# Kernel tuning notes

Measured on AMD Instinct MI355X. Metric: run time of the kernel, lower is better.

The kernel has to match this reference:

```python
import jax, jax.numpy as jnp
import numpy as np

N = 50000      # nodes
E = 200000     # edges per edge type (avg in-degree 16 over 4 etypes)
R = 4          # number of edge types
DIN = 128
DH = 128
DOUT = 64


def setup_inputs() -> dict:
    key = jax.random.key(0)
    ks = jax.random.split(key, 6)
    feat = jax.random.normal(ks[0], (N, DIN), dtype=jnp.float32)
    edges = jax.random.randint(ks[1], (R, 2, E), 0, N)  # [R, (src,dst), E]
    s1 = 1.0 / np.sqrt(DIN)
    W1 = jax.random.uniform(ks[2], (R, DIN, DH), jnp.float32, -s1, s1)
    b1 = jax.random.uniform(ks[3], (R, DH), jnp.float32, -s1, s1)
    s2 = 1.0 / np.sqrt(DH)
    W2 = jax.random.uniform(ks[4], (R, DH, DOUT), jnp.float32, -s2, s2)
    b2 = jax.random.uniform(ks[5], (R, DOUT), jnp.float32, -s2, s2)
    return {"feat": feat, "W1": W1, "b1": b1, "W2": W2, "b2": b2, "edges": edges}


def _hetero_layer(h, W, b, edges):
    """Per-etype Linear -> copy_u + mean over in-edges -> sum across etypes."""
    n = h.shape[0]

    def per_etype(Wr, br, er):
        Wh = h @ Wr + br                       # [N, d_out]
        src, dst = er[0], er[1]
        msg = Wh[src]                          # gather [E, d_out]
        ssum = jax.ops.segment_sum(msg, dst, num_segments=n)
        deg = jax.ops.segment_sum(jnp.ones((er.shape[1],), Wh.dtype), dst,
                                  num_segments=n)
        return ssum / jnp.maximum(deg, 1.0)[:, None]   # mean; 0 for isolated nodes

    return jax.vmap(per_etype)(W, b, edges).sum(axis=0)  # 'sum' cross reducer


def reference(feat, W1, b1, W2, b2, edges):
    h = _hetero_layer(feat, W1, b1, edges)
    h = jax.nn.relu(h)
    return _hetero_layer(h, W2, b2, edges)
```

## Files before the change

### kernel.cpp

```cpp
#include <hip/hip_runtime.h>

#define NN 50000
#define EE 200000
#define RR 4
#define SC_TOTAL (RR * NN)
#define CAP 32
#define GTILE ((NN + 127) / 128)
#define NB_G1 (4 * GTILE)
#define NB_F  1563

typedef __attribute__((ext_vector_type(8))) short bf16x8;
typedef __attribute__((ext_vector_type(4))) float f32x4;

__device__ inline unsigned short f2bf(float x) {
    unsigned int u = __float_as_uint(x);
    u += 0x7fffu + ((u >> 16) & 1u);
    return (unsigned short)(u >> 16);
}
__device__ inline float bflo(unsigned u) { return __uint_as_float(u << 16); }
__device__ inline float bfhi(unsigned u) { return __uint_as_float(u & 0xffff0000u); }

__global__ __launch_bounds__(256) void init_kernel(
    const float* __restrict__ feat, unsigned short* __restrict__ featb,
    const float* __restrict__ W1, const float* __restrict__ b1,
    const float* __restrict__ W2, const float* __restrict__ b2,
    unsigned short* __restrict__ W1T, unsigned short* __restrict__ W2T,
    float* __restrict__ btab1, float* __restrict__ btab2,
    int* __restrict__ cnt)
{
    int b = blockIdx.x, t = threadIdx.x;
    if (b < 6250) {
        int i = (b * 256 + t) * 4;
        float4 v = *(const float4*)&feat[i];
        unsigned lo = (unsigned)f2bf(v.x) | ((unsigned)f2bf(v.y) << 16);
        unsigned hi = (unsigned)f2bf(v.z) | ((unsigned)f2bf(v.w) << 16);
        *(uint2*)&featb[i] = make_uint2(lo, hi);
    } else if (b < 6506) {
        int i = (b - 6250) * 256 + t;
        int jout = i >> 7, k = i & 127;
        int r = jout >> 7, j = jout & 127;
        W1T[i] = f2bf(W1[r * 16384 + k * 128 + j]);
    } else if (b < 6634) {
        int i = (b - 6506) * 256 + t;
        int jout = i >> 7, k = i & 127;
        int r = jout >> 6, j = jout & 63;
        W2T[i] = f2bf(W2[r * 8192 + k * 64 + j]);
    } else if (b < 6642) {
        int i = (b - 6634) * 256 + t;
        int mm = i >> 7, c = i & 127;
        float s = 0.f;
        #pragma unroll
        for (int r = 0; r < RR; ++r) if (mm & (1 << r)) s += b1[r * 128 + c];
        btab1[i] = s;
    } else if (b < 6646) {
        int i = (b - 6642) * 256 + t;
        int mm = i >> 6, c = i & 63;
        float s = 0.f;
        #pragma unroll
        for (int r = 0; r < RR; ++r) if (mm & (1 << r)) s += b2[r * 64 + c];
        btab2[i] = s;
    } else {
        int i = ((b - 6646) * 256 + t) * 4;
        if (i < SC_TOTAL) *(int4*)&cnt[i] = make_int4(0, 0, 0, 0);
    }
}

__global__ __launch_bounds__(256) void fill_gemm1(
    const int* __restrict__ edges, int* __restrict__ cnt,
    unsigned short* __restrict__ ssrc2,
    const unsigned short* __restrict__ A, const unsigned short* __restrict__ WT,
    unsigned short* __restrict__ H)
{
    __shared__ __align__(16) unsigned short Wl[128 * 128];
    const int bid = blockIdx.x;
    const int tid = threadIdx.x;

    if (bid & 1) {
        int f = bid >> 1;
        #pragma unroll
        for (int k = 0; k < 2; ++k) {
            int i = f * 512 + k * 256 + tid;
            if (i < RR * EE) {
                int r = i / EE;
                int e = i - r * EE;
                const int* es = edges + (size_t)r * 2 * EE;
                int src = es[e];
                int dst = es[EE + e];
                int seg = r * NN + dst;
                int p = atomicAdd(&cnt[seg], 1);
                if (p < CAP) ssrc2[(size_t)seg * CAP + p] = (unsigned short)src;
            }
        }
        return;
    }

    const int g    = bid >> 1;
    const int wv   = tid >> 6;
    const int lane = tid & 63;
    const int m    = lane & 15;
    const int q    = lane >> 4;
    const int col0 = (g & 3) * 128;
    const int row0 = (g >> 2) * 128;

    #pragma unroll
    for (int i = 0; i < 8; ++i) {
        int L  = i * 4096 + tid * 16;
        int nr = L >> 8, ir = L & 255;
        uint4 v = *(const uint4*)((const char*)WT + ((size_t)(col0 + nr) << 8) + ir);
        *(uint4*)((char*)Wl + nr * 256 + (ir ^ ((nr & 7) << 4))) = v;
    }
    __syncthreads();

    f32x4 acc[2][8];
    #pragma unroll
    for (int rf = 0; rf < 2; ++rf)
        #pragma unroll
        for (int nt = 0; nt < 8; ++nt) acc[rf][nt] = (f32x4){0.f, 0.f, 0.f, 0.f};

    const int ra0 = row0 + wv * 32 + m;
    const int ra1 = ra0 + 16;
    const bool g0 = ra0 < NN, g1 = ra1 < NN;
    const unsigned short* Ap0 = A + (size_t)ra0 * 128 + q * 8;
    const unsigned short* Ap1 = A + (size_t)ra1 * 128 + q * 8;
    const bf16x8 bz = (bf16x8){0, 0, 0, 0, 0, 0, 0, 0};

    #pragma unroll
    for (int kk = 0; kk < 4; ++kk) {
        bf16x8 a0 = g0 ? *(const bf16x8*)(Ap0 + kk * 32) : bz;
        bf16x8 a1 = g1 ? *(const bf16x8*)(Ap1 + kk * 32) : bz;
        #pragma unroll
        for (int nt = 0; nt < 8; ++nt) {
            int offb = (nt * 16 + m) * 256 + ((kk * 64 + q * 16) ^ ((m & 7) << 4));
            bf16x8 bfr = *(const bf16x8*)((const char*)Wl + offb);
            acc[0][nt] = __builtin_amdgcn_mfma_f32_16x16x32_bf16(a0, bfr, acc[0][nt], 0, 0, 0);
            acc[1][nt] = __builtin_amdgcn_mfma_f32_16x16x32_bf16(a1, bfr, acc[1][nt], 0, 0, 0);
        }
    }

    #pragma unroll
    for (int rf = 0; rf < 2; ++rf) {
        #pragma unroll
        for (int rg = 0; rg < 4; ++rg) {
            int row = row0 + wv * 32 + rf * 16 + q * 4 + rg;
            if (row < NN) {
                unsigned short* Hp = H + (size_t)row * 512 + col0 + m;
                #pragma unroll
                for (int nt = 0; nt < 8; ++nt)
                    Hp[nt * 16] = f2bf(acc[rf][nt][rg]);
            }
        }
    }
}

template<int OTOT>
__global__ __launch_bounds__(256) void gemm_tf(
    const unsigned short* __restrict__ A, const unsigned short* __restrict__ WT,
    unsigned short* __restrict__ H)
{
    __shared__ __align__(16) unsigned short Wl[128 * 128];
    const int tid  = threadIdx.x;
    const int wv   = tid >> 6;
    const int lane = tid & 63;
    const int m    = lane & 15;
    const int q    = lane >> 4;
    const int col0 = blockIdx.x * 128;
    const int row0 = blockIdx.y * 128;

    #pragma unroll
    for (int i = 0; i < 8; ++i) {
        int L  = i * 4096 + tid * 16;
        int nr = L >> 8, ir = L & 255;
        uint4 v = *(const uint4*)((const char*)WT + ((size_t)(col0 + nr) << 8) + ir);
        *(uint4*)((char*)Wl + nr * 256 + (ir ^ ((nr & 7) << 4))) = v;
    }
    __syncthreads();

    f32x4 acc[2][8];
    #pragma unroll
    for (int rf = 0; rf < 2; ++rf)
        #pragma unroll
        for (int nt = 0; nt < 8; ++nt) acc[rf][nt] = (f32x4){0.f, 0.f, 0.f, 0.f};

    const int ra0 = row0 + wv * 32 + m;
    const int ra1 = ra0 + 16;
    const bool g0 = ra0 < NN, g1 = ra1 < NN;
    const unsigned short* Ap0 = A + (size_t)ra0 * 128 + q * 8;
    const unsigned short* Ap1 = A + (size_t)ra1 * 128 + q * 8;
    const bf16x8 bz = (bf16x8){0, 0, 0, 0, 0, 0, 0, 0};

    #pragma unroll
    for (int kk = 0; kk < 4; ++kk) {
        bf16x8 a0 = g0 ? *(const bf16x8*)(Ap0 + kk * 32) : bz;
        bf16x8 a1 = g1 ? *(const bf16x8*)(Ap1 + kk * 32) : bz;
        #pragma unroll
        for (int nt = 0; nt < 8; ++nt) {
            int offb = (nt * 16 + m) * 256 + ((kk * 64 + q * 16) ^ ((m & 7) << 4));
            bf16x8 bfr = *(const bf16x8*)((const char*)Wl + offb);
            acc[0][nt] = __builtin_amdgcn_mfma_f32_16x16x32_bf16(a0, bfr, acc[0][nt], 0, 0, 0);
            acc[1][nt] = __builtin_amdgcn_mfma_f32_16x16x32_bf16(a1, bfr, acc[1][nt], 0, 0, 0);
        }
    }

    #pragma unroll
    for (int rf = 0; rf < 2; ++rf) {
        #pragma unroll
        for (int rg = 0; rg < 4; ++rg) {
            int row = row0 + wv * 32 + rf * 16 + q * 4 + rg;
            if (row < NN) {
                unsigned short* Hp = H + (size_t)row * OTOT + col0 + m;
                #pragma unroll
                for (int nt = 0; nt < 8; ++nt)
                    Hp[nt * 16] = f2bf(acc[rf][nt][rg]);
            }
        }
    }
}

__global__ __launch_bounds__(256) void gather_node1(
    const unsigned short* __restrict__ H1, const unsigned short* __restrict__ ssrc2,
    const int* __restrict__ cnt, const float* __restrict__ btab1,
    unsigned short* __restrict__ h1r)
{
    int n = blockIdx.x * 16 + (threadIdx.x >> 4);
    if (n >= NN) return;
    int l = threadIdx.x & 15;
    float a0 = 0.f, a1 = 0.f, a2 = 0.f, a3 = 0.f, a4 = 0.f, a5 = 0.f, a6 = 0.f, a7 = 0.f;
    int mk = 0;
    #pragma unroll
    for (int r = 0; r < RR; ++r) {
        int seg = r * NN + n;
        int deg = cnt[seg];
        if (deg <= 0) continue;
        mk |= 1 << r;
        int nd = (deg < CAP) ? deg : CAP;
        const unsigned short* lst  = ssrc2 + (size_t)seg * CAP;
        const unsigned short* base = H1 + r * 128 + l * 8;
        float b0 = 0.f, b1v = 0.f, b2v = 0.f, b3 = 0.f, b4 = 0.f, b5 = 0.f, b6 = 0.f, b7 = 0.f;
        int j = 0;
        for (; j + 1 < nd; j += 2) {
            uint4 u0 = *(const uint4*)(base + (size_t)lst[j] * 512);
            uint4 u1 = *(const uint4*)(base + (size_t)lst[j + 1] * 512);
            b0 += bflo(u0.x) + bflo(u1.x); b1v += bfhi(u0.x) + bfhi(u1.x);
            b2v += bflo(u0.y) + bflo(u1.y); b3 += bfhi(u0.y) + bfhi(u1.y);
            b4 += bflo(u0.z) + bflo(u1.z); b5 += bfhi(u0.z) + bfhi(u1.z);
            b6 += bflo(u0.w) + bflo(u1.w); b7 += bfhi(u0.w) + bfhi(u1.w);
        }
        if (j < nd) {
            uint4 u0 = *(const uint4*)(base + (size_t)lst[j] * 512);
            b0 += bflo(u0.x); b1v += bfhi(u0.x);
            b2v += bflo(u0.y); b3 += bfhi(u0.y);
            b4 += bflo(u0.z); b5 += bfhi(u0.z);
            b6 += bflo(u0.w); b7 += bfhi(u0.w);
        }
        float inv = 1.0f / (float)deg;
        a0 += b0 * inv; a1 += b1v * inv; a2 += b2v * inv; a3 += b3 * inv;
        a4 += b4 * inv; a5 += b5 * inv; a6 += b6 * inv; a7 += b7 * inv;
    }
    const float* bt = btab1 + mk * 128 + l * 8;
    float4 t0 = *(const float4*)bt;
    float4 t1 = *(const float4*)(bt + 4);
    uint4 o;
    o.x = (unsigned)f2bf(fmaxf(a0 + t0.x, 0.f)) | ((unsigned)f2bf(fmaxf(a1 + t0.y, 0.f)) << 16);
    o.y = (unsigned)f2bf(fmaxf(a2 + t0.z, 0.f)) | ((unsigned)f2bf(fmaxf(a3 + t0.w, 0.f)) << 16);
    o.z = (unsigned)f2bf(fmaxf(a4 + t1.x, 0.f)) | ((unsigned)f2bf(fmaxf(a5 + t1.y, 0.f)) << 16);
    o.w = (unsigned)f2bf(fmaxf(a6 + t1.z, 0.f)) | ((unsigned)f2bf(fmaxf(a7 + t1.w, 0.f)) << 16);
    *(uint4*)&h1r[(size_t)n * 128 + l * 8] = o;
}

__global__ __launch_bounds__(256) void gather_node2(
    const unsigned short* __restrict__ H2, const unsigned short* __restrict__ ssrc2,
    const int* __restrict__ cnt, const float* __restrict__ btab2,
    float* __restrict__ out)
{
    int n = blockIdx.x * 32 + (threadIdx.x >> 3);
    if (n >= NN) return;
    int l = threadIdx.x & 7;
    float a0 = 0.f, a1 = 0.f, a2 = 0.f, a3 = 0.f, a4 = 0.f, a5 = 0.f, a6 = 0.f, a7 = 0.f;
    int mk = 0;
    #pragma unroll
    for (int r = 0; r < RR; ++r) {
        int seg = r * NN + n;
        int deg = cnt[seg];
        if (deg <= 0) continue;
        mk |= 1 << r;
        int nd = (deg < CAP) ? deg : CAP;
        const unsigned short* lst  = ssrc2 + (size_t)seg * CAP;
        const unsigned short* base = H2 + r * 64 + l * 8;
        float b0 = 0.f, b1v = 0.f, b2v = 0.f, b3 = 0.f, b4 = 0.f, b5 = 0.f, b6 = 0.f, b7 = 0.f;
        int j = 0;
        for (; j + 1 < nd; j += 2) {
            uint4 u0 = *(const uint4*)(base + (size_t)lst[j] * 256);
            uint4 u1 = *(const uint4*)(base + (size_t)lst[j + 1] * 256);
            b0 += bflo(u0.x) + bflo(u1.x); b1v += bfhi(u0.x) + bfhi(u1.x);
            b2v += bflo(u0.y) + bflo(u1.y); b3 += bfhi(u0.y) + bfhi(u1.y);
            b4 += bflo(u0.z) + bflo(u1.z); b5 += bfhi(u0.z) + bfhi(u1.z);
            b6 += bflo(u0.w) + bflo(u1.w); b7 += bfhi(u0.w) + bfhi(u1.w);
        }
        if (j < nd) {
            uint4 u0 = *(const uint4*)(base + (size_t)lst[j] * 256);
            b0 += bflo(u0.x); b1v += bfhi(u0.x);
            b2v += bflo(u0.y); b3 += bfhi(u0.y);
            b4 += bflo(u0.z); b5 += bfhi(u0.z);
            b6 += bflo(u0.w); b7 += bfhi(u0.w);
        }
        float inv = 1.0f / (float)deg;
        a0 += b0 * inv; a1 += b1v * inv; a2 += b2v * inv; a3 += b3 * inv;
        a4 += b4 * inv; a5 += b5 * inv; a6 += b6 * inv; a7 += b7 * inv;
    }
    const float* bt = btab2 + mk * 64 + l * 8;
    float4 t0 = *(const float4*)bt;
    float4 t1 = *(const float4*)(bt + 4);
    float* op = out + (size_t)n * 64 + l * 8;
    *(float4*)op       = make_float4(a0 + t0.x, a1 + t0.y, a2 + t0.z, a3 + t0.w);
    *(float4*)(op + 4) = make_float4(a4 + t1.x, a5 + t1.y, a6 + t1.z, a7 + t1.w);
}

extern "C" void kernel_launch(void* const* d_in, const int* in_sizes, int n_in,
                              void* d_out, int out_size, void* d_ws, size_t ws_size,
                              hipStream_t stream)
{
    const float* feat  = (const float*)d_in[0];
    const float* W1    = (const float*)d_in[1];
    const float* b1    = (const float*)d_in[2];
    const float* W2    = (const float*)d_in[3];
    const float* b2    = (const float*)d_in[4];
    const int*   edges = (const int*)d_in[5];
    float* out = (float*)d_out;

    char* p = (char*)d_ws;
    auto alloc = [&](size_t bytes) { char* q = p; p += (bytes + 255) & ~(size_t)255; return q; };
    int* cnt                 = (int*)alloc((size_t)SC_TOTAL * 4);
    unsigned short* ssrc2    = (unsigned short*)alloc((size_t)SC_TOTAL * CAP * 2);
    unsigned short* W1T      = (unsigned short*)alloc((size_t)512 * 128 * 2);
    unsigned short* W2T      = (unsigned short*)alloc((size_t)256 * 128 * 2);
    float* btab1             = (float*)alloc((size_t)16 * 128 * 4);
    float* btab2             = (float*)alloc((size_t)16 * 64 * 4);
    unsigned short* featb    = (unsigned short*)alloc((size_t)NN * 128 * 2);
    unsigned short* h1r      = (unsigned short*)alloc((size_t)NN * 128 * 2);
    unsigned short* H        = (unsigned short*)alloc((size_t)NN * 512 * 2);

    init_kernel<<<6842, 256, 0, stream>>>(feat, featb, W1, b1, W2, b2,
                                          W1T, W2T, btab1, btab2, cnt);
    fill_gemm1<<<NB_G1 + NB_F, 256, 0, stream>>>(edges, cnt, ssrc2, featb, W1T, H);
    gather_node1<<<(NN + 15) / 16, 256, 0, stream>>>(H, ssrc2, cnt, btab1, h1r);
    gemm_tf<256><<<dim3(2, GTILE), 256, 0, stream>>>(h1r, W2T, H);
    gather_node2<<<(NN + 31) / 32, 256, 0, stream>>>(H, ssrc2, cnt, btab2, out);
}
```

Measured before the change: 200.2 us.

## Fuse feat bf16 conversion into GEMM1 and batch-prefetch neighbor indices in gathers

Drops the separate fp32-to-bf16 pass over feat in init_kernel. The first GEMM now loads fp32 rows directly and packs them to bf16 in registers, which removes a full write and re-read of a 12.8MB buffer. The gather kernels now load each node's first 8 neighbor indices per edge type as one uint4 and issue the gathers for all four edge types in an interleaved unrolled loop, to expose more memory-level parallelism. A slower fallback loop handles degrees above 8, and the per-type accumulators raise register pressure.

```diff
diff --git a/kernel.cpp b/kernel.cpp
--- a/kernel.cpp
+++ b/kernel.cpp
@@ -20,8 +20,16 @@
 __device__ inline float bflo(unsigned u) { return __uint_as_float(u << 16); }
 __device__ inline float bfhi(unsigned u) { return __uint_as_float(u & 0xffff0000u); }
 
+__device__ inline bf16x8 pk8(float4 x, float4 y) {
+    bf16x8 o;
+    o[0] = (short)f2bf(x.x); o[1] = (short)f2bf(x.y);
+    o[2] = (short)f2bf(x.z); o[3] = (short)f2bf(x.w);
+    o[4] = (short)f2bf(y.x); o[5] = (short)f2bf(y.y);
+    o[6] = (short)f2bf(y.z); o[7] = (short)f2bf(y.w);
+    return o;
+}
+
 __global__ __launch_bounds__(256) void init_kernel(
-    const float* __restrict__ feat, unsigned short* __restrict__ featb,
     const float* __restrict__ W1, const float* __restrict__ b1,
     const float* __restrict__ W2, const float* __restrict__ b2,
     unsigned short* __restrict__ W1T, unsigned short* __restrict__ W2T,
@@ -29,38 +37,32 @@
     int* __restrict__ cnt)
 {
     int b = blockIdx.x, t = threadIdx.x;
-    if (b < 6250) {
-        int i = (b * 256 + t) * 4;
-        float4 v = *(const float4*)&feat[i];
-        unsigned lo = (unsigned)f2bf(v.x) | ((unsigned)f2bf(v.y) << 16);
-        unsigned hi = (unsigned)f2bf(v.z) | ((unsigned)f2bf(v.w) << 16);
-        *(uint2*)&featb[i] = make_uint2(lo, hi);
-    } else if (b < 6506) {
-        int i = (b - 6250) * 256 + t;
+    if (b < 256) {
+        int i = b * 256 + t;
         int jout = i >> 7, k = i & 127;
         int r = jout >> 7, j = jout & 127;
         W1T[i] = f2bf(W1[r * 16384 + k * 128 + j]);
-    } else if (b < 6634) {
-        int i = (b - 6506) * 256 + t;
+    } else if (b < 384) {
+        int i = (b - 256) * 256 + t;
         int jout = i >> 7, k = i & 127;
         int r = jout >> 6, j = jout & 63;
         W2T[i] = f2bf(W2[r * 8192 + k * 64 + j]);
-    } else if (b < 6642) {
-        int i = (b - 6634) * 256 + t;
+    } else if (b < 392) {
+        int i = (b - 384) * 256 + t;
         int mm = i >> 7, c = i & 127;
         float s = 0.f;
         #pragma unroll
         for (int r = 0; r < RR; ++r) if (mm & (1 << r)) s += b1[r * 128 + c];
         btab1[i] = s;
-    } else if (b < 6646) {
-        int i = (b - 6642) * 256 + t;
+    } else if (b < 396) {
+        int i = (b - 392) * 256 + t;
         int mm = i >> 6, c = i & 63;
         float s = 0.f;
         #pragma unroll
         for (int r = 0; r < RR; ++r) if (mm & (1 << r)) s += b2[r * 64 + c];
         btab2[i] = s;
     } else {
-        int i = ((b - 6646) * 256 + t) * 4;
+        int i = ((b - 396) * 256 + t) * 4;
         if (i < SC_TOTAL) *(int4*)&cnt[i] = make_int4(0, 0, 0, 0);
     }
 }
@@ -68,7 +70,7 @@
 __global__ __launch_bounds__(256) void fill_gemm1(
     const int* __restrict__ edges, int* __restrict__ cnt,
     unsigned short* __restrict__ ssrc2,
-    const unsigned short* __restrict__ A, const unsigned short* __restrict__ WT,
+    const float* __restrict__ feat, const unsigned short* __restrict__ WT,
     unsigned short* __restrict__ H)
 {
     __shared__ __align__(16) unsigned short Wl[128 * 128];
@@ -120,14 +122,23 @@
     const int ra0 = row0 + wv * 32 + m;
     const int ra1 = ra0 + 16;
     const bool g0 = ra0 < NN, g1 = ra1 < NN;
-    const unsigned short* Ap0 = A + (size_t)ra0 * 128 + q * 8;
-    const unsigned short* Ap1 = A + (size_t)ra1 * 128 + q * 8;
+    const float* Af0 = feat + (size_t)ra0 * 128 + q * 8;
+    const float* Af1 = feat + (size_t)ra1 * 128 + q * 8;
     const bf16x8 bz = (bf16x8){0, 0, 0, 0, 0, 0, 0, 0};
 
     #pragma unroll
     for (int kk = 0; kk < 4; ++kk) {
-        bf16x8 a0 = g0 ? *(const bf16x8*)(Ap0 + kk * 32) : bz;
-        bf16x8 a1 = g1 ? *(const bf16x8*)(Ap1 + kk * 32) : bz;
+        bf16x8 a0 = bz, a1 = bz;
+        if (g0) {
+            float4 x = *(const float4*)(Af0 + kk * 32);
+            float4 y = *(const float4*)(Af0 + kk * 32 + 4);
+            a0 = pk8(x, y);
+        }
+        if (g1) {
+            float4 x = *(const float4*)(Af1 + kk * 32);
+            float4 y = *(const float4*)(Af1 + kk * 32 + 4);
+            a1 = pk8(x, y);
+        }
         #pragma unroll
         for (int nt = 0; nt < 8; ++nt) {
             int offb = (nt * 16 + m) * 256 + ((kk * 64 + q * 16) ^ ((m & 7) << 4));
@@ -224,46 +235,74 @@
     int n = blockIdx.x * 16 + (threadIdx.x >> 4);
     if (n >= NN) return;
     int l = threadIdx.x & 15;
-    float a0 = 0.f, a1 = 0.f, a2 = 0.f, a3 = 0.f, a4 = 0.f, a5 = 0.f, a6 = 0.f, a7 = 0.f;
-    int mk = 0;
+
+    int   dg[RR];
+    uint4 id[RR];
     #pragma unroll
     for (int r = 0; r < RR; ++r) {
         int seg = r * NN + n;
-        int deg = cnt[seg];
-        if (deg <= 0) continue;
-        mk |= 1 << r;
-        int nd = (deg < CAP) ? deg : CAP;
-        const unsigned short* lst  = ssrc2 + (size_t)seg * CAP;
-        const unsigned short* base = H1 + r * 128 + l * 8;
-        float b0 = 0.f, b1v = 0.f, b2v = 0.f, b3 = 0.f, b4 = 0.f, b5 = 0.f, b6 = 0.f, b7 = 0.f;
-        int j = 0;
-        for (; j + 1 < nd; j += 2) {
-            uint4 u0 = *(const uint4*)(base + (size_t)lst[j] * 512);
-            uint4 u1 = *(const uint4*)(base + (size_t)lst[j + 1] * 512);
-            b0 += bflo(u0.x) + bflo(u1.x); b1v += bfhi(u0.x) + bfhi(u1.x);
-            b2v += bflo(u0.y) + bflo(u1.y); b3 += bfhi(u0.y) + bfhi(u1.y);
-            b4 += bflo(u0.z) + bflo(u1.z); b5 += bfhi(u0.z) + bfhi(u1.z);
-            b6 += bflo(u0.w) + bflo(u1.w); b7 += bfhi(u0.w) + bfhi(u1.w);
-        }
-        if (j < nd) {
-            uint4 u0 = *(const uint4*)(base + (size_t)lst[j] * 512);
-            b0 += bflo(u0.x); b1v += bfhi(u0.x);
-            b2v += bflo(u0.y); b3 += bfhi(u0.y);
-            b4 += bflo(u0.z); b5 += bfhi(u0.z);
-            b6 += bflo(u0.w); b7 += bfhi(u0.w);
-        }
-        float inv = 1.0f / (float)deg;
-        a0 += b0 * inv; a1 += b1v * inv; a2 += b2v * inv; a3 += b3 * inv;
-        a4 += b4 * inv; a5 += b5 * inv; a6 += b6 * inv; a7 += b7 * inv;
-    }
+        dg[r] = cnt[seg];
+        id[r] = *(const uint4*)(ssrc2 + (size_t)seg * CAP);
+    }
+
+    float ac[RR][8];
+    #pragma unroll
+    for (int r = 0; r < RR; ++r)
+        #pragma unroll
+        for (int i = 0; i < 8; ++i) ac[r][i] = 0.f;
+
+    #pragma unroll
+    for (int j = 0; j < 8; ++j) {
+        #pragma unroll
+        for (int r = 0; r < RR; ++r) {
+            if (j < dg[r]) {
+                unsigned w = (j >> 1) == 0 ? id[r].x : (j >> 1) == 1 ? id[r].y
+                           : (j >> 1) == 2 ? id[r].z : id[r].w;
+                unsigned s = (j & 1) ? (w >> 16) : (w & 0xffffu);
+                uint4 u = *(const uint4*)(H1 + r * 128 + l * 8 + (size_t)s * 512);
+                ac[r][0] += bflo(u.x); ac[r][1] += bfhi(u.x);
+                ac[r][2] += bflo(u.y); ac[r][3] += bfhi(u.y);
+                ac[r][4] += bflo(u.z); ac[r][5] += bfhi(u.z);
+                ac[r][6] += bflo(u.w); ac[r][7] += bfhi(u.w);
+            }
+        }
+    }
+    if ((dg[0] | dg[1] | dg[2] | dg[3]) > 8) {
+        #pragma unroll
+        for (int r = 0; r < RR; ++r) {
+            int nd = dg[r] < CAP ? dg[r] : CAP;
+            for (int j = 8; j < nd; ++j) {
+                unsigned s = ssrc2[(size_t)(r * NN + n) * CAP + j];
+                uint4 u = *(const uint4*)(H1 + r * 128 + l * 8 + (size_t)s * 512);
+                ac[r][0] += bflo(u.x); ac[r][1] += bfhi(u.x);
+                ac[r][2] += bflo(u.y); ac[r][3] += bfhi(u.y);
+                ac[r][4] += bflo(u.z); ac[r][5] += bfhi(u.z);
+                ac[r][6] += bflo(u.w); ac[r][7] += bfhi(u.w);
+            }
+        }
+    }
+
+    int mk = (dg[0] > 0 ? 1 : 0) | (dg[1] > 0 ? 2 : 0) |
+             (dg[2] > 0 ? 4 : 0) | (dg[3] > 0 ? 8 : 0);
+    float iv[RR];
+    #pragma unroll
+    for (int r = 0; r < RR; ++r) iv[r] = dg[r] > 0 ? 1.0f / (float)dg[r] : 0.f;
+
     const float* bt = btab1 + mk * 128 + l * 8;
     float4 t0 = *(const float4*)bt;
     float4 t1 = *(const float4*)(bt + 4);
+    float o0[8] = {t0.x, t0.y, t0.z, t0.w, t1.x, t1.y, t1.z, t1.w};
+    #pragma unroll
+    for (int i = 0; i < 8; ++i) {
+        #pragma unroll
+        for (int r = 0; r < RR; ++r) o0[i] += ac[r][i] * iv[r];
+        o0[i] = fmaxf(o0[i], 0.f);
+    }
     uint4 o;
-    o.x = (unsigned)f2bf(fmaxf(a0 + t0.x, 0.f)) | ((unsigned)f2bf(fmaxf(a1 + t0.y, 0.f)) << 16);
-    o.y = (unsigned)f2bf(fmaxf(a2 + t0.z, 0.f)) | ((unsigned)f2bf(fmaxf(a3 + t0.w, 0.f)) << 16);
-    o.z = (unsigned)f2bf(fmaxf(a4 + t1.x, 0.f)) | ((unsigned)f2bf(fmaxf(a5 + t1.y, 0.f)) << 16);
-    o.w = (unsigned)f2bf(fmaxf(a6 + t1.z, 0.f)) | ((unsigned)f2bf(fmaxf(a7 + t1.w, 0.f)) << 16);
+    o.x = (unsigned)f2bf(o0[0]) | ((unsigned)f2bf(o0[1]) << 16);
+    o.y = (unsigned)f2bf(o0[2]) | ((unsigned)f2bf(o0[3]) << 16);
+    o.z = (unsigned)f2bf(o0[4]) | ((unsigned)f2bf(o0[5]) << 16);
+    o.w = (unsigned)f2bf(o0[6]) | ((unsigned)f2bf(o0[7]) << 16);
     *(uint4*)&h1r[(size_t)n * 128 + l * 8] = o;
 }
 
@@ -275,44 +314,71 @@
     int n = blockIdx.x * 32 + (threadIdx.x >> 3);
     if (n >= NN) return;
     int l = threadIdx.x & 7;
-    float a0 = 0.f, a1 = 0.f, a2 = 0.f, a3 = 0.f, a4 = 0.f, a5 = 0.f, a6 = 0.f, a7 = 0.f;
-    int mk = 0;
+
+    int   dg[RR];
+    uint4 id[RR];
     #pragma unroll
     for (int r = 0; r < RR; ++r) {
         int seg = r * NN + n;
-        int deg = cnt[seg];
-        if (deg <= 0) continue;
-        mk |= 1 << r;
-        int nd = (deg < CAP) ? deg : CAP;
-        const unsigned short* lst  = ssrc2 + (size_t)seg * CAP;
-        const unsigned short* base = H2 + r * 64 + l * 8;
-        float b0 = 0.f, b1v = 0.f, b2v = 0.f, b3 = 0.f, b4 = 0.f, b5 = 0.f, b6 = 0.f, b7 = 0.f;
-        int j = 0;
-        for (; j + 1 < nd; j += 2) {
-            uint4 u0 = *(const uint4*)(base + (size_t)lst[j] * 256);
-            uint4 u1 = *(const uint4*)(base + (size_t)lst[j + 1] * 256);
-            b0 += bflo(u0.x) + bflo(u1.x); b1v += bfhi(u0.x) + bfhi(u1.x);
-            b2v += bflo(u0.y) + bflo(u1.y); b3 += bfhi(u0.y) + bfhi(u1.y);
-            b4 += bflo(u0.z) + bflo(u1.z); b5 += bfhi(u0.z) + bfhi(u1.z);
-            b6 += bflo(u0.w) + bflo(u1.w); b7 += bfhi(u0.w) + bfhi(u1.w);
-        }
-        if (j < nd) {
-            uint4 u0 = *(const uint4*)(base + (size_t)lst[j] * 256);
-            b0 += bflo(u0.x); b1v += bfhi(u0.x);
-            b2v += bflo(u0.y); b3 += bfhi(u0.y);
-            b4 += bflo(u0.z); b5 += bfhi(u0.z);
-            b6 += bflo(u0.w); b7 += bfhi(u0.w);
-        }
-        float inv = 1.0f / (float)deg;
-        a0 += b0 * inv; a1 += b1v * inv; a2 += b2v * inv; a3 += b3 * inv;
-        a4 += b4 * inv; a5 += b5 * inv; a6 += b6 * inv; a7 += b7 * inv;
-    }
+        dg[r] = cnt[seg];
+        id[r] = *(const uint4*)(ssrc2 + (size_t)seg * CAP);
+    }
+
+    float ac[RR][8];
+    #pragma unroll
+    for (int r = 0; r < RR; ++r)
+        #pragma unroll
+        for (int i = 0; i < 8; ++i) ac[r][i] = 0.f;
+
+    #pragma unroll
+    for (int j = 0; j < 8; ++j) {
+        #pragma unroll
+        for (int r = 0; r < RR; ++r) {
+            if (j < dg[r]) {
+                unsigned w = (j >> 1) == 0 ? id[r].x : (j >> 1) == 1 ? id[r].y
+                           : (j >> 1) == 2 ? id[r].z : id[r].w;
+                unsigned s = (j & 1) ? (w >> 16) : (w & 0xffffu);
+                uint4 u = *(const uint4*)(H2 + r * 64 + l * 8 + (size_t)s * 256);
+                ac[r][0] += bflo(u.x); ac[r][1] += bfhi(u.x);
+                ac[r][2] += bflo(u.y); ac[r][3] += bfhi(u.y);
+                ac[r][4] += bflo(u.z); ac[r][5] += bfhi(u.z);
+                ac[r][6] += bflo(u.w); ac[r][7] += bfhi(u.w);
+            }
+        }
+    }
+    if ((dg[0] | dg[1] | dg[2] | dg[3]) > 8) {
+        #pragma unroll
+        for (int r = 0; r < RR; ++r) {
+            int nd = dg[r] < CAP ? dg[r] : CAP;
+            for (int j = 8; j < nd; ++j) {
+                unsigned s = ssrc2[(size_t)(r * NN + n) * CAP + j];
+                uint4 u = *(const uint4*)(H2 + r * 64 + l * 8 + (size_t)s * 256);
+                ac[r][0] += bflo(u.x); ac[r][1] += bfhi(u.x);
+                ac[r][2] += bflo(u.y); ac[r][3] += bfhi(u.y);
+                ac[r][4] += bflo(u.z); ac[r][5] += bfhi(u.z);
+                ac[r][6] += bflo(u.w); ac[r][7] += bfhi(u.w);
+            }
+        }
+    }
+
+    int mk = (dg[0] > 0 ? 1 : 0) | (dg[1] > 0 ? 2 : 0) |
+             (dg[2] > 0 ? 4 : 0) | (dg[3] > 0 ? 8 : 0);
+    float iv[RR];
+    #pragma unroll
+    for (int r = 0; r < RR; ++r) iv[r] = dg[r] > 0 ? 1.0f / (float)dg[r] : 0.f;
+
     const float* bt = btab2 + mk * 64 + l * 8;
     float4 t0 = *(const float4*)bt;
     float4 t1 = *(const float4*)(bt + 4);
+    float o0[8] = {t0.x, t0.y, t0.z, t0.w, t1.x, t1.y, t1.z, t1.w};
+    #pragma unroll
+    for (int i = 0; i < 8; ++i)
+        #pragma unroll
+        for (int r = 0; r < RR; ++r) o0[i] += ac[r][i] * iv[r];
+
     float* op = out + (size_t)n * 64 + l * 8;
-    *(float4*)op       = make_float4(a0 + t0.x, a1 + t0.y, a2 + t0.z, a3 + t0.w);
-    *(float4*)(op + 4) = make_float4(a4 + t1.x, a5 + t1.y, a6 + t1.z, a7 + t1.w);
+    *(float4*)op       = make_float4(o0[0], o0[1], o0[2], o0[3]);
+    *(float4*)(op + 4) = make_float4(o0[4], o0[5], o0[6], o0[7]);
 }
 
 extern "C" void kernel_launch(void* const* d_in, const int* in_sizes, int n_in,
@@ -335,13 +401,12 @@
     unsigned short* W2T      = (unsigned short*)alloc((size_t)256 * 128 * 2);
     float* btab1             = (float*)alloc((size_t)16 * 128 * 4);
     float* btab2             = (float*)alloc((size_t)16 * 64 * 4);
-    unsigned short* featb    = (unsigned short*)alloc((size_t)NN * 128 * 2);
     unsigned short* h1r      = (unsigned short*)alloc((size_t)NN * 128 * 2);
     unsigned short* H        = (unsigned short*)alloc((size_t)NN * 512 * 2);
 
-    init_kernel<<<6842, 256, 0, stream>>>(feat, featb, W1, b1, W2, b2,
-                                          W1T, W2T, btab1, btab2, cnt);
-    fill_gemm1<<<NB_G1 + NB_F, 256, 0, stream>>>(edges, cnt, ssrc2, featb, W1T, H);
+    init_kernel<<<592, 256, 0, stream>>>(W1, b1, W2, b2,
+                                         W1T, W2T, btab1, btab2, cnt);
+    fill_gemm1<<<NB_G1 + NB_F, 256, 0, stream>>>(edges, cnt, ssrc2, feat, W1T, H);
     gather_node1<<<(NN + 15) / 16, 256, 0, stream>>>(H, ssrc2, cnt, btab1, h1r);
     gemm_tf<256><<<dim3(2, GTILE), 256, 0, stream>>>(h1r, W2T, H);
     gather_node2<<<(NN + 31) / 32, 256, 0, stream>>>(H, ssrc2, cnt, btab2, out);
```

Result: slower. 220.5 us (+10.1%).

## Fuse layer-1 gather/mean/relu with layer-2 GEMM via shared-memory tile

Applied to the files above, without the earlier changes.

Replaces the separate gather_node1 kernel and the second GEMM with a single kernel. Each block gathers and mean-aggregates 64 nodes into a swizzled LDS tile, then runs MFMA against W2T read directly from global memory. This removes the h1r round trip through global memory and one launch. In exchange, W2T fragments are reloaded from global or L2 by every block rather than staged in LDS, and the GEMM phase is serialized behind the irregular gather within each block.

```diff
diff --git a/kernel.cpp b/kernel.cpp
--- a/kernel.cpp
+++ b/kernel.cpp
@@ -17,6 +17,9 @@
     u += 0x7fffu + ((u >> 16) & 1u);
     return (unsigned short)(u >> 16);
 }
+__device__ inline unsigned pk2(float a, float b) {
+    return (unsigned)f2bf(a) | ((unsigned)f2bf(b) << 16);
+}
 __device__ inline float bflo(unsigned u) { return __uint_as_float(u << 16); }
 __device__ inline float bfhi(unsigned u) { return __uint_as_float(u & 0xffff0000u); }
 
@@ -32,9 +35,7 @@
     if (b < 6250) {
         int i = (b * 256 + t) * 4;
         float4 v = *(const float4*)&feat[i];
-        unsigned lo = (unsigned)f2bf(v.x) | ((unsigned)f2bf(v.y) << 16);
-        unsigned hi = (unsigned)f2bf(v.z) | ((unsigned)f2bf(v.w) << 16);
-        *(uint2*)&featb[i] = make_uint2(lo, hi);
+        *(uint2*)&featb[i] = make_uint2(pk2(v.x, v.y), pk2(v.z, v.w));
     } else if (b < 6506) {
         int i = (b - 6250) * 256 + t;
         int jout = i >> 7, k = i & 127;
@@ -152,119 +153,110 @@
     }
 }
 
-template<int OTOT>
-__global__ __launch_bounds__(256) void gemm_tf(
-    const unsigned short* __restrict__ A, const unsigned short* __restrict__ WT,
-    unsigned short* __restrict__ H)
-{
-    __shared__ __align__(16) unsigned short Wl[128 * 128];
-    const int tid  = threadIdx.x;
+__global__ __launch_bounds__(256) void gather_gemm2(
+    const unsigned short* __restrict__ H1, const unsigned short* __restrict__ ssrc2,
+    const int* __restrict__ cnt, const float* __restrict__ btab1,
+    const unsigned short* __restrict__ W2T, unsigned short* __restrict__ H2)
+{
+    __shared__ __align__(16) unsigned short Al[64 * 128];
+    const int tid = threadIdx.x;
+    const int n0  = blockIdx.x * 64;
+
+    const int l  = tid & 15;
+    const int ng = tid >> 4;
+    #pragma unroll
+    for (int pass = 0; pass < 4; ++pass) {
+        int nl = pass * 16 + ng;
+        int n  = n0 + nl;
+        float a0 = 0.f, a1 = 0.f, a2 = 0.f, a3 = 0.f,
+              a4 = 0.f, a5 = 0.f, a6 = 0.f, a7 = 0.f;
+        int mk = 0;
+        if (n < NN) {
+            #pragma unroll
+            for (int r = 0; r < RR; ++r) {
+                int seg = r * NN + n;
+                int deg = cnt[seg];
+                if (deg <= 0) continue;
+                mk |= 1 << r;
+                int nd = (deg < CAP) ? deg : CAP;
+                const unsigned short* lst  = ssrc2 + (size_t)seg * CAP;
+                const unsigned short* base = H1 + r * 128 + l * 8;
+                float b0 = 0.f, b1v = 0.f, b2v = 0.f, b3 = 0.f,
+                      b4 = 0.f, b5 = 0.f, b6 = 0.f, b7 = 0.f;
+                int j = 0;
+                for (; j + 1 < nd; j += 2) {
+                    uint4 u0 = *(const uint4*)(base + (size_t)lst[j] * 512);
+                    uint4 u1 = *(const uint4*)(base + (size_t)lst[j + 1] * 512);
+                    b0 += bflo(u0.x) + bflo(u1.x); b1v += bfhi(u0.x) + bfhi(u1.x);
+                    b2v += bflo(u0.y) + bflo(u1.y); b3 += bfhi(u0.y) + bfhi(u1.y);
+                    b4 += bflo(u0.z) + bflo(u1.z); b5 += bfhi(u0.z) + bfhi(u1.z);
+                    b6 += bflo(u0.w) + bflo(u1.w); b7 += bfhi(u0.w) + bfhi(u1.w);
+                }
+                if (j < nd) {
+                    uint4 u0 = *(const uint4*)(base + (size_t)lst[j] * 512);
+                    b0 += bflo(u0.x); b1v += bfhi(u0.x);
+                    b2v += bflo(u0.y); b3 += bfhi(u0.y);
+                    b4 += bflo(u0.z); b5 += bfhi(u0.z);
+                    b6 += bflo(u0.w); b7 += bfhi(u0.w);
+                }
+                float inv = 1.0f / (float)deg;
+                a0 += b0 * inv; a1 += b1v * inv; a2 += b2v * inv; a3 += b3 * inv;
+                a4 += b4 * inv; a5 += b5 * inv; a6 += b6 * inv; a7 += b7 * inv;
+            }
+        }
+        const float* bt = btab1 + mk * 128 + l * 8;
+        float4 t0 = *(const float4*)bt;
+        float4 t1 = *(const float4*)(bt + 4);
+        uint4 o;
+        o.x = pk2(fmaxf(a0 + t0.x, 0.f), fmaxf(a1 + t0.y, 0.f));
+        o.y = pk2(fmaxf(a2 + t0.z, 0.f), fmaxf(a3 + t0.w, 0.f));
+        o.z = pk2(fmaxf(a4 + t1.x, 0.f), fmaxf(a5 + t1.y, 0.f));
+        o.w = pk2(fmaxf(a6 + t1.z, 0.f), fmaxf(a7 + t1.w, 0.f));
+        int sw = (nl & 7) << 4;
+        *(uint4*)((char*)Al + ((nl * 256 + l * 16) ^ sw)) = o;
+    }
+    __syncthreads();
+
+    const int lane = tid & 63;
     const int wv   = tid >> 6;
-    const int lane = tid & 63;
     const int m    = lane & 15;
     const int q    = lane >> 4;
-    const int col0 = blockIdx.x * 128;
-    const int row0 = blockIdx.y * 128;
-
-    #pragma unroll
-    for (int i = 0; i < 8; ++i) {
-        int L  = i * 4096 + tid * 16;
-        int nr = L >> 8, ir = L & 255;
-        uint4 v = *(const uint4*)((const char*)WT + ((size_t)(col0 + nr) << 8) + ir);
-        *(uint4*)((char*)Wl + nr * 256 + (ir ^ ((nr & 7) << 4))) = v;
-    }
-    __syncthreads();
-
-    f32x4 acc[2][8];
-    #pragma unroll
-    for (int rf = 0; rf < 2; ++rf)
-        #pragma unroll
-        for (int nt = 0; nt < 8; ++nt) acc[rf][nt] = (f32x4){0.f, 0.f, 0.f, 0.f};
-
-    const int ra0 = row0 + wv * 32 + m;
-    const int ra1 = ra0 + 16;
-    const bool g0 = ra0 < NN, g1 = ra1 < NN;
-    const unsigned short* Ap0 = A + (size_t)ra0 * 128 + q * 8;
-    const unsigned short* Ap1 = A + (size_t)ra1 * 128 + q * 8;
-    const bf16x8 bz = (bf16x8){0, 0, 0, 0, 0, 0, 0, 0};
-
-    #pragma unroll
-    for (int kk = 0; kk < 4; ++kk) {
-        bf16x8 a0 = g0 ? *(const bf16x8*)(Ap0 + kk * 32) : bz;
-        bf16x8 a1 = g1 ? *(const bf16x8*)(Ap1 + kk * 32) : bz;
-        #pragma unroll
-        for (int nt = 0; nt < 8; ++nt) {
-            int offb = (nt * 16 + m) * 256 + ((kk * 64 + q * 16) ^ ((m & 7) << 4));
-            bf16x8 bfr = *(const bf16x8*)((const char*)Wl + offb);
-            acc[0][nt] = __builtin_amdgcn_mfma_f32_16x16x32_bf16(a0, bfr, acc[0][nt], 0, 0, 0);
-            acc[1][nt] = __builtin_amdgcn_mfma_f32_16x16x32_bf16(a1, bfr, acc[1][nt], 0, 0, 0);
-        }
-    }
-
-    #pragma unroll
-    for (int rf = 0; rf < 2; ++rf) {
+
+    bf16x8 af[4];
+    {
+        int row = wv * 16 + m;
+        int sw  = (row & 7) << 4;
+        #pragma unroll
+        for (int kk = 0; kk < 4; ++kk)
+            af[kk] = *(const bf16x8*)((const char*)Al +
+                         ((row * 256 + kk * 64 + q * 16) ^ sw));
+    }
+
+    #pragma unroll
+    for (int cp = 0; cp < 2; ++cp) {
+        f32x4 acc[8];
+        #pragma unroll
+        for (int nt = 0; nt < 8; ++nt) acc[nt] = (f32x4){0.f, 0.f, 0.f, 0.f};
+        #pragma unroll
+        for (int kk = 0; kk < 4; ++kk) {
+            #pragma unroll
+            for (int nt = 0; nt < 8; ++nt) {
+                bf16x8 bfr = *(const bf16x8*)(W2T +
+                    (size_t)(cp * 128 + nt * 16 + m) * 128 + kk * 32 + q * 8);
+                acc[nt] = __builtin_amdgcn_mfma_f32_16x16x32_bf16(af[kk], bfr, acc[nt], 0, 0, 0);
+            }
+        }
         #pragma unroll
         for (int rg = 0; rg < 4; ++rg) {
-            int row = row0 + wv * 32 + rf * 16 + q * 4 + rg;
+            int row = n0 + wv * 16 + q * 4 + rg;
             if (row < NN) {
-                unsigned short* Hp = H + (size_t)row * OTOT + col0 + m;
+                unsigned short* Hp = H2 + (size_t)row * 256 + cp * 128 + m;
                 #pragma unroll
                 for (int nt = 0; nt < 8; ++nt)
-                    Hp[nt * 16] = f2bf(acc[rf][nt][rg]);
-            }
-        }
-    }
-}
-
-__global__ __launch_bounds__(256) void gather_node1(
-    const unsigned short* __restrict__ H1, const unsigned short* __restrict__ ssrc2,
-    const int* __restrict__ cnt, const float* __restrict__ btab1,
-    unsigned short* __restrict__ h1r)
-{
-    int n = blockIdx.x * 16 + (threadIdx.x >> 4);
-    if (n >= NN) return;
-    int l = threadIdx.x & 15;
-    float a0 = 0.f, a1 = 0.f, a2 = 0.f, a3 = 0.f, a4 = 0.f, a5 = 0.f, a6 = 0.f, a7 = 0.f;
-    int mk = 0;
-    #pragma unroll
-    for (int r = 0; r < RR; ++r) {
-        int seg = r * NN + n;
-        int deg = cnt[seg];
-        if (deg <= 0) continue;
-        mk |= 1 << r;
-        int nd = (deg < CAP) ? deg : CAP;
-        const unsigned short* lst  = ssrc2 + (size_t)seg * CAP;
-        const unsigned short* base = H1 + r * 128 + l * 8;
-        float b0 = 0.f, b1v = 0.f, b2v = 0.f, b3 = 0.f, b4 = 0.f, b5 = 0.f, b6 = 0.f, b7 = 0.f;
-        int j = 0;
-        for (; j + 1 < nd; j += 2) {
-            uint4 u0 = *(const uint4*)(base + (size_t)lst[j] * 512);
-            uint4 u1 = *(const uint4*)(base + (size_t)lst[j + 1] * 512);
-            b0 += bflo(u0.x) + bflo(u1.x); b1v += bfhi(u0.x) + bfhi(u1.x);
-            b2v += bflo(u0.y) + bflo(u1.y); b3 += bfhi(u0.y) + bfhi(u1.y);
-            b4 += bflo(u0.z) + bflo(u1.z); b5 += bfhi(u0.z) + bfhi(u1.z);
-            b6 += bflo(u0.w) + bflo(u1.w); b7 += bfhi(u0.w) + bfhi(u1.w);
-        }
-        if (j < nd) {
-            uint4 u0 = *(const uint4*)(base + (size_t)lst[j] * 512);
-            b0 += bflo(u0.x); b1v += bfhi(u0.x);
-            b2v += bflo(u0.y); b3 += bfhi(u0.y);
-            b4 += bflo(u0.z); b5 += bfhi(u0.z);
-            b6 += bflo(u0.w); b7 += bfhi(u0.w);
-        }
-        float inv = 1.0f / (float)deg;
-        a0 += b0 * inv; a1 += b1v * inv; a2 += b2v * inv; a3 += b3 * inv;
-        a4 += b4 * inv; a5 += b5 * inv; a6 += b6 * inv; a7 += b7 * inv;
-    }
-    const float* bt = btab1 + mk * 128 + l * 8;
-    float4 t0 = *(const float4*)bt;
-    float4 t1 = *(const float4*)(bt + 4);
-    uint4 o;
-    o.x = (unsigned)f2bf(fmaxf(a0 + t0.x, 0.f)) | ((unsigned)f2bf(fmaxf(a1 + t0.y, 0.f)) << 16);
-    o.y = (unsigned)f2bf(fmaxf(a2 + t0.z, 0.f)) | ((unsigned)f2bf(fmaxf(a3 + t0.w, 0.f)) << 16);
-    o.z = (unsigned)f2bf(fmaxf(a4 + t1.x, 0.f)) | ((unsigned)f2bf(fmaxf(a5 + t1.y, 0.f)) << 16);
-    o.w = (unsigned)f2bf(fmaxf(a6 + t1.z, 0.f)) | ((unsigned)f2bf(fmaxf(a7 + t1.w, 0.f)) << 16);
-    *(uint4*)&h1r[(size_t)n * 128 + l * 8] = o;
+                    Hp[nt * 16] = f2bf(acc[nt][rg]);
+            }
+        }
+    }
 }
 
 __global__ __launch_bounds__(256) void gather_node2(
@@ -275,7 +267,8 @@
     int n = blockIdx.x * 32 + (threadIdx.x >> 3);
     if (n >= NN) return;
     int l = threadIdx.x & 7;
-    float a0 = 0.f, a1 = 0.f, a2 = 0.f, a3 = 0.f, a4 = 0.f, a5 = 0.f, a6 = 0.f, a7 = 0.f;
+    float a0 = 0.f, a1 = 0.f, a2 = 0.f, a3 = 0.f,
+          a4 = 0.f, a5 = 0.f, a6 = 0.f, a7 = 0.f;
     int mk = 0;
     #pragma unroll
     for (int r = 0; r < RR; ++r) {
@@ -286,7 +279,8 @@
         int nd = (deg < CAP) ? deg : CAP;
         const unsigned short* lst  = ssrc2 + (size_t)seg * CAP;
         const unsigned short* base = H2 + r * 64 + l * 8;
-        float b0 = 0.f, b1v = 0.f, b2v = 0.f, b3 = 0.f, b4 = 0.f, b5 = 0.f, b6 = 0.f, b7 = 0.f;
+        float b0 = 0.f, b1v = 0.f, b2v = 0.f, b3 = 0.f,
+              b4 = 0.f, b5 = 0.f, b6 = 0.f, b7 = 0.f;
         int j = 0;
         for (; j + 1 < nd; j += 2) {
             uint4 u0 = *(const uint4*)(base + (size_t)lst[j] * 256);
@@ -336,13 +330,12 @@
     float* btab1             = (float*)alloc((size_t)16 * 128 * 4);
     float* btab2             = (float*)alloc((size_t)16 * 64 * 4);
     unsigned short* featb    = (unsigned short*)alloc((size_t)NN * 128 * 2);
-    unsigned short* h1r      = (unsigned short*)alloc((size_t)NN * 128 * 2);
     unsigned short* H        = (unsigned short*)alloc((size_t)NN * 512 * 2);
+    unsigned short* H2       = (unsigned short*)alloc((size_t)NN * 256 * 2);
 
     init_kernel<<<6842, 256, 0, stream>>>(feat, featb, W1, b1, W2, b2,
                                           W1T, W2T, btab1, btab2, cnt);
     fill_gemm1<<<NB_G1 + NB_F, 256, 0, stream>>>(edges, cnt, ssrc2, featb, W1T, H);
-    gather_node1<<<(NN + 15) / 16, 256, 0, stream>>>(H, ssrc2, cnt, btab1, h1r);
-    gemm_tf<256><<<dim3(2, GTILE), 256, 0, stream>>>(h1r, W2T, H);
-    gather_node2<<<(NN + 31) / 32, 256, 0, stream>>>(H, ssrc2, cnt, btab2, out);
-}
+    gather_gemm2<<<(NN + 63) / 64, 256, 0, stream>>>(H, ssrc2, cnt, btab1, W2T, H2);
+    gather_node2<<<(NN + 31) / 32, 256, 0, stream>>>(H2, ssrc2, cnt, btab2, out);
+}
```

Result: slower. 229.9 us (+14.8%).
